# Performance work log

Measured on AMD Instinct MI355X. Metric: run time of the kernel, lower is better.

## Reference

```python
import jax, jax.numpy as jnp
import numpy as np

B, S, D, H = 4, 2048, 1024, 16
HD = D // H

def setup_inputs() -> dict:
    key = jax.random.key(0)
    ks = jax.random.split(key, 5)
    x = jax.random.normal(ks[0], (B, S, D), dtype=jnp.float32)
    mask = jnp.ones((B, S), dtype=jnp.int32)
    # torch nn.Linear init scale ~ 1/sqrt(fan_in); use small normal for stability
    qkv_w = jax.random.normal(ks[1], (3 * D, D), dtype=jnp.float32) * (1.0 / np.sqrt(D))
    qkv_b = jax.random.normal(ks[2], (3 * D,), dtype=jnp.float32) * 0.02
    out_w = jax.random.normal(ks[3], (D, D), dtype=jnp.float32) * (1.0 / np.sqrt(D))
    out_b = jax.random.normal(ks[4], (D,), dtype=jnp.float32) * 0.02
    return {"x": x, "mask": mask, "qkv_w": qkv_w, "qkv_b": qkv_b,
            "out_w": out_w, "out_b": out_b}

def reference(x, mask, qkv_w, qkv_b, out_w, out_b):
    b, s, d = x.shape
    scale = np.sqrt(HD).astype(np.float32)
    # qkv projection: torch Linear y = x @ W^T + b
    qkv = x @ qkv_w.T + qkv_b                      # (b, s, 3d)
    qkv = qkv.reshape(b, s, 3, H, HD)
    qkv = jnp.transpose(qkv, (2, 0, 3, 1, 4))      # (3, b, H, s, hd)
    q, k, v = qkv[0], qkv[1], qkv[2]
    scores = jnp.einsum('bhqd,bhkd->bhqk', q, k) / scale  # (b, H, s, s)
    neg_inf = jnp.float32(-jnp.inf)
    causal = jnp.tril(jnp.ones((s, s), dtype=bool))
    scores = jnp.where(causal[None, None], scores, neg_inf)
    key_mask = (mask != 0)[:, None, None, :]       # (b, 1, 1, s)
    scores = jnp.where(key_mask, scores, neg_inf)
    attn = jax.nn.softmax(scores, axis=-1)
    out = jnp.einsum('bhqk,bhkd->bhqd', attn, v)   # (b, H, s, hd)
    out = jnp.transpose(out, (0, 2, 1, 3)).reshape(b, s, d)
    return out @ out_w.T + out_b
```

## Files before the change

kernel.cpp:

```cpp
#include <hip/hip_runtime.h>
#include <stdint.h>
#include <type_traits>

#define BB  4
#define SS  2048
#define DD  1024
#define HH  16
#define HDD 64

typedef __attribute__((ext_vector_type(8))) short s16x8;
typedef __attribute__((ext_vector_type(4))) float f32x4;

__device__ inline short f2bf(float f) {
    union { float f; unsigned int u; } v; v.f = f;
    unsigned int r = (v.u + 0x7fffu + ((v.u >> 16) & 1u)) >> 16;
    return (short)r;
}

__device__ inline float bf2f(short s) {
    union { unsigned int u; float f; } v;
    v.u = ((unsigned int)(unsigned short)s) << 16;
    return v.f;
}

#define GLL(gp, lp) __builtin_amdgcn_global_load_lds( \
    (const __attribute__((address_space(1))) void*)(gp), \
    (__attribute__((address_space(3))) void*)(lp), 16, 0, 0)

__device__ inline void lds_barrier() {
    asm volatile("s_waitcnt lgkmcnt(0)" ::: "memory");
    __builtin_amdgcn_sched_barrier(0);
    __builtin_amdgcn_s_barrier();
    __builtin_amdgcn_sched_barrier(0);
}

__global__ void cvt_kernel(const float* __restrict__ src, short* __restrict__ dst, int n) {
    int i = (blockIdx.x * 256 + threadIdx.x) * 8;
    if (i >= n) return;
    const float4* s = (const float4*)(src + i);
    float4 a = s[0], b = s[1];
    s16x8 o;
    o[0]=f2bf(a.x); o[1]=f2bf(a.y); o[2]=f2bf(a.z); o[3]=f2bf(a.w);
    o[4]=f2bf(b.x); o[5]=f2bf(b.y); o[6]=f2bf(b.z); o[7]=f2bf(b.w);
    *(s16x8*)(dst + i) = o;
}

template<int EPI>
__global__ __launch_bounds__(256)
void gemm_bt(const short* __restrict__ A, const short* __restrict__ Bw,
             const float* __restrict__ bias, float* __restrict__ Cf,
             short* __restrict__ Qo, short* __restrict__ Ko, short* __restrict__ Vo,
             int M, int N, int K)
{
    __shared__ short lsA[128 * 32];
    __shared__ short lsB[128 * 32];
    const int tid  = threadIdx.x;
    const int w    = tid >> 6, lane = tid & 63;
    const int quad = lane >> 4, l15 = lane & 15;
    const int m0 = blockIdx.x * 128, n0 = blockIdx.y * 128;
    const int mw = (w & 1) * 64, nw = (w >> 1) * 64;

    f32x4 acc[4][4] = {};

    const int srow = w * 32 + (lane >> 2);
    const int scol = (lane & 3) * 8;
    const short* pA = A + (size_t)(m0 + srow) * K + scol;
    const short* pB = Bw + (size_t)(n0 + srow) * K + scol;
    short* lAbase0 = &lsA[(w * 32) * 32];
    short* lAbase1 = &lsA[(w * 32 + 16) * 32];
    short* lBbase0 = &lsB[(w * 32) * 32];
    short* lBbase1 = &lsB[(w * 32 + 16) * 32];

    for (int kk = 0; kk < K; kk += 32) {
        __syncthreads();
        GLL(pA + kk,            lAbase0);
        GLL(pA + kk + 16 * K,   lAbase1);
        GLL(pB + kk,            lBbase0);
        GLL(pB + kk + 16 * K,   lBbase1);
        asm volatile("s_waitcnt vmcnt(0)" ::: "memory");
        __syncthreads();

        s16x8 af[4], bfr[4];
        for (int t = 0; t < 4; ++t) {
            af[t]  = *(const s16x8*)&lsA[(mw + t * 16 + l15) * 32 + quad * 8];
            bfr[t] = *(const s16x8*)&lsB[(nw + t * 16 + l15) * 32 + quad * 8];
        }
        for (int i = 0; i < 4; ++i)
            for (int j = 0; j < 4; ++j)
                acc[i][j] = __builtin_amdgcn_mfma_f32_16x16x32_bf16(af[i], bfr[j], acc[i][j], 0, 0, 0);
    }

    if (EPI == 0) {
        for (int i = 0; i < 4; ++i) {
            int row = m0 + mw + i * 16 + quad * 4;
            for (int j = 0; j < 4; ++j) {
                int col = n0 + nw + j * 16 + l15;
                float bv = bias[col];
                for (int r = 0; r < 4; ++r)
                    Cf[(size_t)(row + r) * N + col] = acc[i][j][r] + bv;
            }
        }
    } else {
        for (int i = 0; i < 4; ++i) {
            int row = m0 + mw + i * 16 + quad * 4;
            for (int j = 0; j < 4; ++j) {
                int col = n0 + nw + j * 16 + l15;
                float bv = bias[col];
                int sel = col >> 10, h = (col >> 6) & 15, hd = col & 63;
                for (int r = 0; r < 4; ++r) {
                    int rr = row + r;
                    int b = rr >> 11, s = rr & 2047;
                    short val = f2bf(acc[i][j][r] + bv);
                    if (sel == 0)      Qo[(((size_t)b * HH + h) * SS + s) * HDD + hd] = val;
                    else if (sel == 1) Ko[(((size_t)b * HH + h) * SS + s) * HDD + hd] = val;
                    else               Vo[(((size_t)b * HH + h) * HDD + hd) * SS + s] = val;
                }
            }
        }
    }
}

__global__ __launch_bounds__(256, 2)
void attn_kernel(const short* __restrict__ Q, const short* __restrict__ Kb,
                 const short* __restrict__ Vb, const int* __restrict__ mask,
                 short* __restrict__ O)
{
    __shared__ short lsK[2][64 * 64];
    __shared__ short lsV[2][64 * 64];
    __shared__ short lsP[4][32 * 64];
    __shared__ short lsM[SS];

    const int tid  = threadIdx.x;
    const int w    = tid >> 6, lane = tid & 63;
    const int quad = lane >> 4, l15 = lane & 15;
    const int bx = blockIdx.x, bh = blockIdx.y;
    const int b = bh >> 4;
    const size_t baseQK = (size_t)bh * SS * HDD;
    const size_t baseV  = (size_t)bh * HDD * SS;
    const float SC = 0.18033688f;
    const int grow = lane >> 3;
    const int gcol = ((lane & 7) ^ grow) * 8;
    const int l7 = l15 & 7;

    {
        const int4* mp = (const int4*)(mask + b * SS);
        int4 a = mp[tid * 2], c = mp[tid * 2 + 1];
        const short NEG = f2bf(-1e30f);
        s16x8 mo;
        mo[0] = a.x ? (short)0 : NEG; mo[1] = a.y ? (short)0 : NEG;
        mo[2] = a.z ? (short)0 : NEG; mo[3] = a.w ? (short)0 : NEG;
        mo[4] = c.x ? (short)0 : NEG; mo[5] = c.y ? (short)0 : NEG;
        mo[6] = c.z ? (short)0 : NEG; mo[7] = c.w ? (short)0 : NEG;
        *(s16x8*)&lsM[tid * 8] = mo;
    }

    auto issue = [&](int kv0, int buf) {
#pragma unroll
        for (int jj = 0; jj < 2; ++jj) {
            int row = w * 16 + jj * 8 + grow;
            GLL(Kb + baseQK + (size_t)(kv0 + row) * HDD + gcol,
                &lsK[buf][(w * 2 + jj) * 512]);
        }
#pragma unroll
        for (int jj = 0; jj < 2; ++jj) {
            int row = w * 16 + jj * 8 + grow;
            GLL(Vb + baseV + (size_t)row * SS + kv0 + gcol,
                &lsV[buf][(w * 2 + jj) * 512]);
        }
    };

    for (int t = 0; t < 2; ++t) {
        const int qb = t ? bx : (15 - bx);
        const int q0 = qb * 128;
        const int qw0 = q0 + w * 32;

        s16x8 aq[2][2];
#pragma unroll
        for (int s = 0; s < 2; ++s)
#pragma unroll
            for (int ks = 0; ks < 2; ++ks)
                aq[s][ks] = *(const s16x8*)(Q + baseQK +
                    (size_t)(qw0 + s * 16 + l15) * HDD + ks * 32 + quad * 8);

        float m_r[2][4], l_r[2][4];
        f32x4 o_acc[2][4] = {};
#pragma unroll
        for (int s = 0; s < 2; ++s)
#pragma unroll
            for (int r = 0; r < 4; ++r) { m_r[s][r] = -1e30f; l_r[s][r] = 0.f; }

        const int ntiles = 2 * qb + 2;

        lds_barrier();
        issue(0, 0);

        auto tile = [&](auto CC, int kv0, int buf, int kvn) {
            constexpr bool CAUS = decltype(CC)::value;

            lds_barrier();
            if (kvn >= 0) issue(kvn, buf ^ 1);

            float madd[4];
#pragma unroll
            for (int nt = 0; nt < 4; ++nt)
                madd[nt] = bf2f(lsM[kv0 + nt * 16 + l15]);

            if (kvn >= 0) asm volatile("s_waitcnt vmcnt(4)" ::: "memory");
            else          asm volatile("s_waitcnt vmcnt(0)" ::: "memory");
            __builtin_amdgcn_sched_barrier(0);
            __builtin_amdgcn_s_barrier();
            __builtin_amdgcn_sched_barrier(0);

            f32x4 sv[2][4];
#pragma unroll
            for (int s = 0; s < 2; ++s)
#pragma unroll
                for (int nt = 0; nt < 4; ++nt) sv[s][nt] = f32x4{};
#pragma unroll
            for (int ks = 0; ks < 2; ++ks)
#pragma unroll
                for (int nt = 0; nt < 4; ++nt) {
                    s16x8 kf = *(const s16x8*)&lsK[buf][(nt * 16 + l15) * 64 +
                                                       (((ks * 4 + quad) ^ l7) * 8)];
#pragma unroll
                    for (int s = 0; s < 2; ++s)
                        sv[s][nt] = __builtin_amdgcn_mfma_f32_16x16x32_bf16(
                                        aq[s][ks], kf, sv[s][nt], 0, 0, 0);
                }

#pragma unroll
            for (int s = 0; s < 2; ++s) {
                const int rowg0 = qw0 + s * 16 + quad * 4;
#pragma unroll
                for (int nt = 0; nt < 4; ++nt) {
                    int colg = kv0 + nt * 16 + l15;
#pragma unroll
                    for (int r = 0; r < 4; ++r) {
                        float scv = sv[s][nt][r] * SC + madd[nt];
                        if (CAUS && colg > rowg0 + r) scv = -1e30f;
                        sv[s][nt][r] = scv;
                    }
                }
            }

            float rm[2][4];
#pragma unroll
            for (int s = 0; s < 2; ++s)
#pragma unroll
                for (int r = 0; r < 4; ++r) {
                    float v = fmaxf(fmaxf(sv[s][0][r], sv[s][1][r]),
                                    fmaxf(sv[s][2][r], sv[s][3][r]));
                    v = fmaxf(v, __shfl_xor(v, 1));
                    v = fmaxf(v, __shfl_xor(v, 2));
                    v = fmaxf(v, __shfl_xor(v, 4));
                    v = fmaxf(v, __shfl_xor(v, 8));
                    rm[s][r] = v;
                }
            float need = rm[0][0] - m_r[0][0];
#pragma unroll
            for (int s = 0; s < 2; ++s)
#pragma unroll
                for (int r = 0; r < 4; ++r)
                    need = fmaxf(need, rm[s][r] - m_r[s][r]);
            if (!__all(need <= 8.0f)) {
#pragma unroll
                for (int s = 0; s < 2; ++s)
#pragma unroll
                    for (int r = 0; r < 4; ++r) {
                        float nm = fmaxf(m_r[s][r], rm[s][r]);
                        float al = __builtin_amdgcn_exp2f(m_r[s][r] - nm);
                        m_r[s][r] = nm;
                        l_r[s][r] *= al;
#pragma unroll
                        for (int ht = 0; ht < 4; ++ht)
                            o_acc[s][ht][r] *= al;
                    }
            }
#pragma unroll
            for (int s = 0; s < 2; ++s)
#pragma unroll
                for (int r = 0; r < 4; ++r) {
                    float rs = 0.f;
#pragma unroll
                    for (int nt = 0; nt < 4; ++nt) {
                        float p = __builtin_amdgcn_exp2f(sv[s][nt][r] - m_r[s][r]);
                        sv[s][nt][r] = p;
                        rs += p;
                    }
                    l_r[s][r] += rs;
                }

            short* lsPw = lsP[w];
#pragma unroll
            for (int s = 0; s < 2; ++s)
#pragma unroll
                for (int nt = 0; nt < 4; ++nt)
#pragma unroll
                    for (int r = 0; r < 4; ++r) {
                        int prow = s * 16 + quad * 4 + r;
                        lsPw[prow * 64 + (((nt * 2 + (l15 >> 3)) ^ (prow & 7)) << 3) + l7]
                            = f2bf(sv[s][nt][r]);
                    }
            asm volatile("s_waitcnt lgkmcnt(0)" ::: "memory");
            __builtin_amdgcn_sched_barrier(0);

            s16x8 ap[2][2];
#pragma unroll
            for (int s = 0; s < 2; ++s)
#pragma unroll
                for (int k2 = 0; k2 < 2; ++k2)
                    ap[s][k2] = *(const s16x8*)&lsPw[(s * 16 + l15) * 64 +
                                                     (((k2 * 4 + quad) ^ l7) << 3)];
#pragma unroll
            for (int ht = 0; ht < 4; ++ht)
#pragma unroll
                for (int k2 = 0; k2 < 2; ++k2) {
                    s16x8 vf = *(const s16x8*)&lsV[buf][(ht * 16 + l15) * 64 +
                                                        (((k2 * 4 + quad) ^ l7) * 8)];
#pragma unroll
                    for (int s = 0; s < 2; ++s)
                        o_acc[s][ht] = __builtin_amdgcn_mfma_f32_16x16x32_bf16(
                                           ap[s][k2], vf, o_acc[s][ht], 0, 0, 0);
                }
        };

        for (int kt = 0; kt < ntiles; ++kt) {
            const int kvn = (kt + 1 < ntiles) ? (kt + 1) * 64 : -1;
            if (kt >= 2 * qb) tile(std::true_type{},  kt * 64, kt & 1, kvn);
            else              tile(std::false_type{}, kt * 64, kt & 1, kvn);
        }

        const int hcol = (bh & 15) * HDD;
#pragma unroll
        for (int s = 0; s < 2; ++s)
#pragma unroll
            for (int r = 0; r < 4; ++r) {
                float ls = l_r[s][r];
                ls += __shfl_xor(ls, 1);
                ls += __shfl_xor(ls, 2);
                ls += __shfl_xor(ls, 4);
                ls += __shfl_xor(ls, 8);
                float inv = 1.0f / ls;
                int srow = qw0 + s * 16 + quad * 4 + r;
                size_t base = ((size_t)b * SS + srow) * DD + hcol;
#pragma unroll
                for (int ht = 0; ht < 4; ++ht)
                    O[base + ht * 16 + l15] = f2bf(o_acc[s][ht][r] * inv);
            }
    }
}

extern "C" void kernel_launch(void* const* d_in, const int* in_sizes, int n_in,
                              void* d_out, int out_size, void* d_ws, size_t ws_size,
                              hipStream_t stream) {
    const float* x     = (const float*)d_in[0];
    const int*   mask  = (const int*)d_in[1];
    const float* qkv_w = (const float*)d_in[2];
    const float* qkv_b = (const float*)d_in[3];
    const float* out_w = (const float*)d_in[4];
    const float* out_b = (const float*)d_in[5];
    float* out = (float*)d_out;

    const size_t M1 = (size_t)BB * SS;
    short* ws  = (short*)d_ws;
    short* xb  = ws;
    short* qwb = xb  + M1 * DD;
    short* owb = qwb + (size_t)3 * DD * DD;
    short* Qb  = owb + (size_t)DD * DD;
    short* Kb  = Qb  + M1 * DD;
    short* Vb  = Kb  + M1 * DD;
    short* Ob  = Vb  + M1 * DD;

    cvt_kernel<<<(int)(M1 * DD / 8 / 256), 256, 0, stream>>>(x, xb, (int)(M1 * DD));
    cvt_kernel<<<3 * DD * DD / 8 / 256, 256, 0, stream>>>(qkv_w, qwb, 3 * DD * DD);
    cvt_kernel<<<DD * DD / 8 / 256, 256, 0, stream>>>(out_w, owb, DD * DD);

    gemm_bt<1><<<dim3(64, 24), 256, 0, stream>>>(xb, qwb, qkv_b, nullptr,
                                                 Qb, Kb, Vb, 8192, 3072, 1024);
    attn_kernel<<<dim3(8, BB * HH), 256, 0, stream>>>(Qb, Kb, Vb, mask, Ob);
    gemm_bt<0><<<dim3(64, 8), 256, 0, stream>>>(Ob, owb, out_b, out,
                                                nullptr, nullptr, nullptr, 8192, 1024, 1024);
}
```

Before: 309.0 us.

## Rewrite projection GEMMs with 128x256 tiles, double-buffered LDS, and XOR swizzle

Replaces the 128x128, K=32 single-buffered GEMM with a 512-thread 128x256 tile kernel that uses K=64 steps and double-buffered LDS. Loads for the next tile are issued before computing the current one. An XOR-swizzled LDS layout avoids bank conflicts, and a 1D grid with block-index swizzle improves L2 locality. The intent is to hide global-load latency, raise MFMA density and cut LDS conflicts. The cost is more LDS per block (96KB) and fewer blocks for the output projection (256 blocks), which may leave CUs underfilled.

```diff
diff --git a/kernel.cpp b/kernel.cpp
--- a/kernel.cpp
+++ b/kernel.cpp
@@ -46,71 +46,111 @@
 }
 
 template<int EPI>
-__global__ __launch_bounds__(256)
-void gemm_bt(const short* __restrict__ A, const short* __restrict__ Bw,
+__global__ __launch_bounds__(512, 2)
+void gemm256(const short* __restrict__ A, const short* __restrict__ Bw,
              const float* __restrict__ bias, float* __restrict__ Cf,
              short* __restrict__ Qo, short* __restrict__ Ko, short* __restrict__ Vo,
-             int M, int N, int K)
+             int M, int N, int K, int nbx)
 {
-    __shared__ short lsA[128 * 32];
-    __shared__ short lsB[128 * 32];
+    __shared__ short lsA[2][128 * 64];
+    __shared__ short lsB[2][256 * 64];
+
     const int tid  = threadIdx.x;
     const int w    = tid >> 6, lane = tid & 63;
     const int quad = lane >> 4, l15 = lane & 15;
-    const int m0 = blockIdx.x * 128, n0 = blockIdx.y * 128;
-    const int mw = (w & 1) * 64, nw = (w >> 1) * 64;
+    const int wm = w >> 2, wn = w & 3;
+    const int cpx = gridDim.x >> 3;
+    const int swz = (blockIdx.x & 7) * cpx + (blockIdx.x >> 3);
+    const int m0 = (swz / nbx) * 128, n0 = (swz % nbx) * 256;
+    const int grow = lane >> 3;
+    const int gcol = ((lane & 7) ^ grow) * 8;
+    const int l7 = l15 & 7;
 
     f32x4 acc[4][4] = {};
 
-    const int srow = w * 32 + (lane >> 2);
-    const int scol = (lane & 3) * 8;
-    const short* pA = A + (size_t)(m0 + srow) * K + scol;
-    const short* pB = Bw + (size_t)(n0 + srow) * K + scol;
-    short* lAbase0 = &lsA[(w * 32) * 32];
-    short* lAbase1 = &lsA[(w * 32 + 16) * 32];
-    short* lBbase0 = &lsB[(w * 32) * 32];
-    short* lBbase1 = &lsB[(w * 32 + 16) * 32];
-
-    for (int kk = 0; kk < K; kk += 32) {
-        __syncthreads();
-        GLL(pA + kk,            lAbase0);
-        GLL(pA + kk + 16 * K,   lAbase1);
-        GLL(pB + kk,            lBbase0);
-        GLL(pB + kk + 16 * K,   lBbase1);
-        asm volatile("s_waitcnt vmcnt(0)" ::: "memory");
-        __syncthreads();
-
-        s16x8 af[4], bfr[4];
-        for (int t = 0; t < 4; ++t) {
-            af[t]  = *(const s16x8*)&lsA[(mw + t * 16 + l15) * 32 + quad * 8];
-            bfr[t] = *(const s16x8*)&lsB[(nw + t * 16 + l15) * 32 + quad * 8];
-        }
-        for (int i = 0; i < 4; ++i)
-            for (int j = 0; j < 4; ++j)
-                acc[i][j] = __builtin_amdgcn_mfma_f32_16x16x32_bf16(af[i], bfr[j], acc[i][j], 0, 0, 0);
+    auto issue = [&](int kt, int buf) {
+#pragma unroll
+        for (int jj = 0; jj < 2; ++jj) {
+            int row = w * 16 + jj * 8 + grow;
+            GLL(A + (size_t)(m0 + row) * K + kt * 64 + gcol,
+                &lsA[buf][(w * 2 + jj) * 512]);
+        }
+#pragma unroll
+        for (int jj = 0; jj < 4; ++jj) {
+            int row = w * 32 + jj * 8 + grow;
+            GLL(Bw + (size_t)(n0 + row) * K + kt * 64 + gcol,
+                &lsB[buf][(w * 4 + jj) * 512]);
+        }
+    };
+
+    const int NT = K >> 6;
+    issue(0, 0);
+    for (int t = 0; t < NT; ++t) {
+        const int buf = t & 1;
+        lds_barrier();
+        if (t + 1 < NT) {
+            issue(t + 1, buf ^ 1);
+            asm volatile("s_waitcnt vmcnt(6)" ::: "memory");
+        } else {
+            asm volatile("s_waitcnt vmcnt(0)" ::: "memory");
+        }
+        __builtin_amdgcn_sched_barrier(0);
+        __builtin_amdgcn_s_barrier();
+        __builtin_amdgcn_sched_barrier(0);
+
+        s16x8 af[4][2], bfr[4][2];
+#pragma unroll
+        for (int mf = 0; mf < 4; ++mf)
+#pragma unroll
+            for (int ks = 0; ks < 2; ++ks)
+                af[mf][ks] = *(const s16x8*)&lsA[buf][(wm * 64 + mf * 16 + l15) * 64 +
+                                                     (((ks * 4 + quad) ^ l7) * 8)];
+#pragma unroll
+        for (int nf = 0; nf < 4; ++nf)
+#pragma unroll
+            for (int ks = 0; ks < 2; ++ks)
+                bfr[nf][ks] = *(const s16x8*)&lsB[buf][(wn * 64 + nf * 16 + l15) * 64 +
+                                                      (((ks * 4 + quad) ^ l7) * 8)];
+
+        __builtin_amdgcn_s_setprio(1);
+#pragma unroll
+        for (int ks = 0; ks < 2; ++ks)
+#pragma unroll
+            for (int mf = 0; mf < 4; ++mf)
+#pragma unroll
+                for (int nf = 0; nf < 4; ++nf)
+                    acc[mf][nf] = __builtin_amdgcn_mfma_f32_16x16x32_bf16(
+                                      af[mf][ks], bfr[nf][ks], acc[mf][nf], 0, 0, 0);
+        __builtin_amdgcn_s_setprio(0);
     }
 
     if (EPI == 0) {
-        for (int i = 0; i < 4; ++i) {
-            int row = m0 + mw + i * 16 + quad * 4;
-            for (int j = 0; j < 4; ++j) {
-                int col = n0 + nw + j * 16 + l15;
+#pragma unroll
+        for (int mf = 0; mf < 4; ++mf) {
+            int row = m0 + wm * 64 + mf * 16 + quad * 4;
+#pragma unroll
+            for (int nf = 0; nf < 4; ++nf) {
+                int col = n0 + wn * 64 + nf * 16 + l15;
                 float bv = bias[col];
+#pragma unroll
                 for (int r = 0; r < 4; ++r)
-                    Cf[(size_t)(row + r) * N + col] = acc[i][j][r] + bv;
+                    Cf[(size_t)(row + r) * N + col] = acc[mf][nf][r] + bv;
             }
         }
     } else {
-        for (int i = 0; i < 4; ++i) {
-            int row = m0 + mw + i * 16 + quad * 4;
-            for (int j = 0; j < 4; ++j) {
-                int col = n0 + nw + j * 16 + l15;
+#pragma unroll
+        for (int mf = 0; mf < 4; ++mf) {
+            int row = m0 + wm * 64 + mf * 16 + quad * 4;
+#pragma unroll
+            for (int nf = 0; nf < 4; ++nf) {
+                int col = n0 + wn * 64 + nf * 16 + l15;
                 float bv = bias[col];
                 int sel = col >> 10, h = (col >> 6) & 15, hd = col & 63;
+#pragma unroll
                 for (int r = 0; r < 4; ++r) {
                     int rr = row + r;
                     int b = rr >> 11, s = rr & 2047;
-                    short val = f2bf(acc[i][j][r] + bv);
+                    short val = f2bf(acc[mf][nf][r] + bv);
                     if (sel == 0)      Qo[(((size_t)b * HH + h) * SS + s) * HDD + hd] = val;
                     else if (sel == 1) Ko[(((size_t)b * HH + h) * SS + s) * HDD + hd] = val;
                     else               Vo[(((size_t)b * HH + h) * HDD + hd) * SS + s] = val;
@@ -375,9 +415,9 @@
     cvt_kernel<<<3 * DD * DD / 8 / 256, 256, 0, stream>>>(qkv_w, qwb, 3 * DD * DD);
     cvt_kernel<<<DD * DD / 8 / 256, 256, 0, stream>>>(out_w, owb, DD * DD);
 
-    gemm_bt<1><<<dim3(64, 24), 256, 0, stream>>>(xb, qwb, qkv_b, nullptr,
-                                                 Qb, Kb, Vb, 8192, 3072, 1024);
+    gemm256<1><<<768, 512, 0, stream>>>(xb, qwb, qkv_b, nullptr,
+                                        Qb, Kb, Vb, 8192, 3072, 1024, 12);
     attn_kernel<<<dim3(8, BB * HH), 256, 0, stream>>>(Qb, Kb, Vb, mask, Ob);
-    gemm_bt<0><<<dim3(64, 8), 256, 0, stream>>>(Ob, owb, out_b, out,
-                                                nullptr, nullptr, nullptr, 8192, 1024, 1024);
-}
+    gemm256<0><<<256, 512, 0, stream>>>(Ob, owb, out_b, out,
+                                        nullptr, nullptr, nullptr, 8192, 1024, 1024, 4);
+}
```

Result: slower. 331.7 us (+7.3%).
